# Kernel tuning notes

Measured on AMD Instinct MI355X. Metric: run time of the kernel, lower is better.

Reference implementation:

```python
import jax, jax.numpy as jnp
import numpy as np

B, S, D_MODEL = 2, 2048, 1024
H, D = 16, 64
D_INNER = H * D
EPS = 1e-5


def setup_inputs() -> dict:
    key = jax.random.key(0)
    ks = jax.random.split(key, 10)
    sc = 0.02
    return {
        "x": jax.random.normal(ks[0], (B, S, D_MODEL), dtype=jnp.float32),
        "Wq": jax.random.normal(ks[1], (D_MODEL, D_INNER), dtype=jnp.float32) * sc,
        "Wk": jax.random.normal(ks[2], (D_MODEL, D_INNER), dtype=jnp.float32) * sc,
        "Wv": jax.random.normal(ks[3], (D_MODEL, D_INNER), dtype=jnp.float32) * sc,
        "Wg": jax.random.normal(ks[4], (D_MODEL, D_INNER), dtype=jnp.float32) * sc,
        "Wa": jax.random.normal(ks[5], (D_MODEL, H), dtype=jnp.float32) * sc,
        "ba": jax.random.normal(ks[6], (H,), dtype=jnp.float32) * sc,
        "Wo": jax.random.normal(ks[7], (D_INNER, D_MODEL), dtype=jnp.float32) * sc,
        "gn_w": jnp.ones((D_INNER,), dtype=jnp.float32),
        "gn_b": jnp.zeros((D_INNER,), dtype=jnp.float32),
    }


def reference(x, Wq, Wk, Wv, Wg, Wa, ba, Wo, gn_w, gn_b):
    b, s, _ = x.shape
    # projections -> [B,H,S,D]
    q = jax.nn.silu(jnp.einsum('bsm,md->bsd', x, Wq).reshape(b, s, H, D).transpose(0, 2, 1, 3))
    k = jax.nn.silu(jnp.einsum('bsm,md->bsd', x, Wk).reshape(b, s, H, D).transpose(0, 2, 1, 3))
    v = jnp.einsum('bsm,md->bsd', x, Wv).reshape(b, s, H, D).transpose(0, 2, 1, 3)

    # data-dependent log forget gate, per head: [B,H,S]
    log_alpha = -jax.nn.softplus(jnp.einsum('bsm,mh->bsh', x, Wa) + ba)
    cum = jnp.cumsum(log_alpha, axis=1).transpose(0, 2, 1)  # [B,H,S]

    # decay[b,h,i,j] = exp(cum[i] - cum[j]) for j <= i, else 0
    diff = cum[:, :, :, None] - cum[:, :, None, :]  # [B,H,S,S]
    causal = jnp.tril(jnp.ones((s, s), dtype=bool))
    decay = jnp.exp(jnp.where(causal, diff, -jnp.inf))

    attn = jnp.einsum('bhid,bhjd->bhij', q, k) * decay
    o = jnp.einsum('bhij,bhjd->bhid', attn, v)  # [B,H,S,D]
    o = o.transpose(0, 2, 1, 3)  # [B,S,H,D]

    # GroupNorm(H groups) over channels-within-group and spatial dim S
    mean = jnp.mean(o, axis=(1, 3), keepdims=True)          # per (b,h)
    var = jnp.var(o, axis=(1, 3), keepdims=True)
    o = (o - mean) / jnp.sqrt(var + EPS)
    o = o * gn_w.reshape(H, D) + gn_b.reshape(H, D)
    o = o.reshape(b, s, H * D)

    gate = jax.nn.sigmoid(jnp.einsum('bsm,md->bsd', x, Wg))
    return jnp.einsum('bsd,dm->bsm', o * gate, Wo)
```

## Files before the change

kernel.cpp:

```cpp
#include <hip/hip_runtime.h>
#include <math.h>
#include <stdint.h>

typedef __attribute__((ext_vector_type(4))) float f32x4;
typedef __attribute__((ext_vector_type(8))) short bf16x8;

constexpr int NB = 2;
constexpr int NS = 2048;
constexpr int NM = 1024;
constexpr int NH = 16;
constexpr int ND = 64;
constexpr int NDI = 1024;

__device__ __forceinline__ float bf2f(unsigned short u) {
  uint32_t x = ((uint32_t)u) << 16; float f; __builtin_memcpy(&f, &x, 4); return f;
}
__device__ __forceinline__ unsigned short f2bf(float f) {
  uint32_t x; __builtin_memcpy(&x, &f, 4);
  x += 0x7FFFu + ((x >> 16) & 1u);
  return (unsigned short)(x >> 16);
}

__global__ __launch_bounds__(256) void k_prep(const float* __restrict__ x,
    const float* __restrict__ w0, const float* __restrict__ w1,
    const float* __restrict__ w2, const float* __restrict__ w3,
    const float* __restrict__ w4, const float* __restrict__ Wa,
    unsigned short* __restrict__ xb,
    unsigned short* __restrict__ t0, unsigned short* __restrict__ t1,
    unsigned short* __restrict__ t2, unsigned short* __restrict__ t3,
    unsigned short* __restrict__ t4, unsigned short* __restrict__ wa_pad) {
  int bid = blockIdx.x;
  if (bid < 2048) {
    int i = bid * 256 + threadIdx.x;
    const float4* p = (const float4*)(x + (size_t)i * 8);
    float4 a = p[0], b = p[1];
    unsigned short r[8] = {f2bf(a.x), f2bf(a.y), f2bf(a.z), f2bf(a.w),
                           f2bf(b.x), f2bf(b.y), f2bf(b.z), f2bf(b.w)};
    *(uint4*)(xb + (size_t)i * 8) = *(const uint4*)r;
  } else if (bid < 7168) {
    __shared__ float tile[32][33];
    int w = bid - 2048;
    int z = w >> 10, within = w & 1023;
    const float* src = z == 0 ? w0 : z == 1 ? w1 : z == 2 ? w2 : z == 3 ? w3 : w4;
    unsigned short* dst = z == 0 ? t0 : z == 1 ? t1 : z == 2 ? t2 : z == 3 ? t3 : t4;
    int c0 = (within & 31) * 32, r0 = (within >> 5) * 32;
    int tx = threadIdx.x & 31, ty = threadIdx.x >> 5;
    #pragma unroll
    for (int i = 0; i < 4; i++)
      tile[ty + i * 8][tx] = src[(size_t)(r0 + ty + i * 8) * 1024 + c0 + tx];
    __syncthreads();
    #pragma unroll
    for (int i = 0; i < 4; i++)
      dst[(size_t)(c0 + ty + i * 8) * 1024 + r0 + tx] = f2bf(tile[tx][ty + i * 8]);
  } else {
    int idx = (bid - 7168) * 256 + threadIdx.x;
    int h = idx >> 10, k2 = idx & 1023;
    wa_pad[idx] = (h < 16) ? f2bf(Wa[k2 * 16 + h]) : (unsigned short)0;
  }
}

__global__ __launch_bounds__(256) void k_la_gemm(const unsigned short* __restrict__ xb,
    const unsigned short* __restrict__ wa_pad, float* __restrict__ la8) {
  __shared__ unsigned short As[128 * 32];
  __shared__ unsigned short Bs[128 * 32];
  int tid = threadIdx.x;
  int row0 = blockIdx.y * 128;
  int kbeg = blockIdx.x * 128;
  float* Cp = la8 + (size_t)blockIdx.x * (32 * 2048);
  int w = tid >> 6, l = tid & 63;
  int wr = w >> 1, wc = w & 1;
  int lr = l & 15, lk = l >> 4;
  f32x4 acc[4] = {};
  for (int k0 = kbeg; k0 < kbeg + 128; k0 += 32) {
    __syncthreads();
    #pragma unroll
    for (int i = 0; i < 2; i++) {
      int idx = tid + i * 256;
      int r = idx >> 2, c = idx & 3;
      int cs = c ^ ((r >> 1) & 3);
      const unsigned short* srcA = xb + (size_t)(row0 + r) * NM + k0 + cs * 8;
      const unsigned short* srcB = wa_pad + (size_t)r * NM + k0 + cs * 8;
      __builtin_amdgcn_global_load_lds(
          (const __attribute__((address_space(1))) void*)srcA,
          (__attribute__((address_space(3))) void*)((char*)As + (w * 64 + i * 256) * 16),
          16, 0, 0);
      __builtin_amdgcn_global_load_lds(
          (const __attribute__((address_space(1))) void*)srcB,
          (__attribute__((address_space(3))) void*)((char*)Bs + (w * 64 + i * 256) * 16),
          16, 0, 0);
    }
    __syncthreads();
    if (wc == 0) {
      bf16x8 b = *(const bf16x8*)&Bs[lr * 32 + (lk ^ ((lr >> 1) & 3)) * 8];
      #pragma unroll
      for (int m = 0; m < 4; m++) {
        int ra = wr * 64 + m * 16 + lr;
        bf16x8 a = *(const bf16x8*)&As[ra * 32 + (lk ^ ((ra >> 1) & 3)) * 8];
        acc[m] = __builtin_amdgcn_mfma_f32_16x16x32_bf16(a, b, acc[m], 0, 0, 0);
      }
    }
  }
  if (wc == 0) {
    #pragma unroll
    for (int m = 0; m < 4; m++) {
      #pragma unroll
      for (int j = 0; j < 4; j++) {
        int row = row0 + wr * 64 + m * 16 + lk * 4 + j;
        int bb = row >> 11, s = row & 2047;
        Cp[((size_t)(bb * 16 + lr)) * 2048 + s] = acc[m][j];
      }
    }
  }
}

__global__ __launch_bounds__(256) void k_cumsum(const float* __restrict__ la8,
    const float* __restrict__ ba, float* __restrict__ cum,
    float* __restrict__ psum, float* __restrict__ psq) {
  int g = blockIdx.x;
  int h = g & 15;
  if (threadIdx.x == 0) { psum[g] = 0.f; psq[g] = 0.f; }
  float bah = ba[h];
  const float* p0 = la8 + (size_t)g * NS;
  float* out = cum + (size_t)g * NS;
  __shared__ float part[256];
  float v[8]; float sum = 0.f;
  int base = threadIdx.x * 8;
  #pragma unroll
  for (int i = 0; i < 8; i++) {
    int s = base + i;
    float z = bah;
    #pragma unroll
    for (int sl = 0; sl < 8; sl++) z += p0[sl * 65536 + s];
    float sp = fmaxf(z, 0.f) + log1pf(expf(-fabsf(z)));
    v[i] = -sp; sum += v[i];
  }
  part[threadIdx.x] = sum;
  __syncthreads();
  for (int off = 1; off < 256; off <<= 1) {
    float add = (threadIdx.x >= off) ? part[threadIdx.x - off] : 0.f;
    __syncthreads();
    part[threadIdx.x] += add;
    __syncthreads();
  }
  float run = (threadIdx.x > 0) ? part[threadIdx.x - 1] : 0.f;
  #pragma unroll
  for (int i = 0; i < 8; i++) { run += v[i]; out[base + i] = run; }
}

__global__ __launch_bounds__(512, 2) void k_proj8(
    const unsigned short* __restrict__ A,
    const unsigned short* __restrict__ Wcat,
    unsigned short* __restrict__ q, unsigned short* __restrict__ k,
    unsigned short* __restrict__ v, unsigned short* __restrict__ g) {
  __shared__ unsigned short Ab[2][256 * 64];
  __shared__ unsigned short Bb[2][256 * 64];
  int tid = threadIdx.x;
  int bid = blockIdx.x;
  int wg = (bid & 7) * 32 + (bid >> 3);
  int bx = wg & 15, by = wg >> 4;
  int row0 = by * 256, col0 = bx * 256;
  int wid = tid >> 6, lane = tid & 63;
  int WR = wid >> 2, WC = wid & 3;
  int lr = lane & 15, lk = lane >> 4;

  auto stage = [&](int kt, int bi) {
    #pragma unroll
    for (int i = 0; i < 4; i++) {
      int idx = tid + i * 512;
      int r = idx >> 3, c = idx & 7;
      int cs = c ^ (r & 7);
      const unsigned short* srcA = A + (size_t)(row0 + r) * NM + kt * 64 + cs * 8;
      __builtin_amdgcn_global_load_lds(
          (const __attribute__((address_space(1))) void*)srcA,
          (__attribute__((address_space(3))) void*)((char*)&Ab[bi][0] + (wid * 64 + i * 512) * 16),
          16, 0, 0);
      const unsigned short* srcB = Wcat + (size_t)(col0 + r) * NM + kt * 64 + cs * 8;
      __builtin_amdgcn_global_load_lds(
          (const __attribute__((address_space(1))) void*)srcB,
          (__attribute__((address_space(3))) void*)((char*)&Bb[bi][0] + (wid * 64 + i * 512) * 16),
          16, 0, 0);
    }
  };

  stage(0, 0);
  stage(1, 1);

  f32x4 acc[8][4] = {};
  for (int kt = 0; kt < 16; ++kt) {
    int bi = kt & 1;
    if (kt < 15) asm volatile("s_waitcnt vmcnt(8)" ::: "memory");
    else         asm volatile("s_waitcnt vmcnt(0)" ::: "memory");
    __builtin_amdgcn_sched_barrier(0);
    __builtin_amdgcn_s_barrier();

    const char* Ap = (const char*)&Ab[bi][0];
    const char* Bp = (const char*)&Bb[bi][0];
    bf16x8 a0[8], b0[4], a1[8], b1[4];
    #pragma unroll
    for (int m = 0; m < 8; m++) {
      int r = WR * 128 + m * 16 + lr;
      a0[m] = *(const bf16x8*)(Ap + r * 128 + ((lk ^ (r & 7)) * 16));
    }
    #pragma unroll
    for (int n = 0; n < 4; n++) {
      int r = WC * 64 + n * 16 + lr;
      b0[n] = *(const bf16x8*)(Bp + r * 128 + ((lk ^ (r & 7)) * 16));
    }
    #pragma unroll
    for (int m = 0; m < 8; m++)
      #pragma unroll
      for (int n = 0; n < 4; n++)
        acc[m][n] = __builtin_amdgcn_mfma_f32_16x16x32_bf16(a0[m], b0[n], acc[m][n], 0, 0, 0);
    #pragma unroll
    for (int m = 0; m < 8; m++) {
      int r = WR * 128 + m * 16 + lr;
      a1[m] = *(const bf16x8*)(Ap + r * 128 + (((lk + 4) ^ (r & 7)) * 16));
    }
    #pragma unroll
    for (int n = 0; n < 4; n++) {
      int r = WC * 64 + n * 16 + lr;
      b1[n] = *(const bf16x8*)(Bp + r * 128 + (((lk + 4) ^ (r & 7)) * 16));
    }
    asm volatile("s_waitcnt lgkmcnt(0)" ::: "memory");
    __builtin_amdgcn_sched_barrier(0);
    __builtin_amdgcn_s_barrier();
    if (kt + 2 < 16) stage(kt + 2, bi);
    __builtin_amdgcn_s_setprio(1);
    #pragma unroll
    for (int m = 0; m < 8; m++)
      #pragma unroll
      for (int n = 0; n < 4; n++)
        acc[m][n] = __builtin_amdgcn_mfma_f32_16x16x32_bf16(a1[m], b1[n], acc[m][n], 0, 0, 0);
    __builtin_amdgcn_s_setprio(0);
  }

  #pragma unroll
  for (int m = 0; m < 8; m++) {
    #pragma unroll
    for (int n = 0; n < 4; n++) {
      int col = col0 + WC * 64 + n * 16 + lr;
      int zone = col >> 10;
      unsigned short* dst = zone == 0 ? q : zone == 1 ? k : zone == 2 ? v : g;
      int cb = col & 1023;
      #pragma unroll
      for (int j = 0; j < 4; j++) {
        int row = row0 + WR * 128 + m * 16 + lk * 4 + j;
        float val = acc[m][n][j];
        if (zone <= 1) val = val / (1.f + expf(-val));
        else if (zone == 3) val = 1.f / (1.f + expf(-val));
        dst[(size_t)row * 1024 + cb] = f2bf(val);
      }
    }
  }
}

__global__ __launch_bounds__(256) void k_out2(const unsigned short* __restrict__ A,
    const unsigned short* __restrict__ Bt, float* __restrict__ C) {
  __shared__ unsigned short As[2][64 * 64];
  __shared__ unsigned short Bs[2][128 * 64];
  int tid = threadIdx.x;
  int bid = blockIdx.x;
  int wg = (bid & 7) * 64 + (bid >> 3);
  int bx = wg & 7, by = wg >> 3;
  int row0 = by * 64, col0 = bx * 128;
  int w = tid >> 6, l = tid & 63;
  int wr = w >> 1, wc = w & 1;
  int lr = l & 15, lk = l >> 4;

  auto stage = [&](int t, int bi) {
    #pragma unroll
    for (int i = 0; i < 2; i++) {
      int idx = tid + i * 256;
      int r = idx >> 3, c = idx & 7;
      int cs = c ^ (r & 7);
      const unsigned short* srcA = A + (size_t)(row0 + r) * NM + t * 64 + cs * 8;
      __builtin_amdgcn_global_load_lds(
          (const __attribute__((address_space(1))) void*)srcA,
          (__attribute__((address_space(3))) void*)((char*)&As[bi][0] + idx * 16),
          16, 0, 0);
    }
    #pragma unroll
    for (int i = 0; i < 4; i++) {
      int idx = tid + i * 256;
      int r = idx >> 3, c = idx & 7;
      int cs = c ^ (r & 7);
      const unsigned short* srcB = Bt + (size_t)(col0 + r) * NM + t * 64 + cs * 8;
      __builtin_amdgcn_global_load_lds(
          (const __attribute__((address_space(1))) void*)srcB,
          (__attribute__((address_space(3))) void*)((char*)&Bs[bi][0] + idx * 16),
          16, 0, 0);
    }
  };

  stage(0, 0);
  asm volatile("s_waitcnt vmcnt(0)" ::: "memory");
  __builtin_amdgcn_s_barrier();

  f32x4 acc[2][4] = {};
  int cur = 0;
  for (int t = 0; t < 16; ++t) {
    if (t < 15) stage(t + 1, cur ^ 1);
    const char* Ap = (const char*)&As[cur][0];
    const char* Bp = (const char*)&Bs[cur][0];
    bf16x8 a[2][2], b[4][2];
    #pragma unroll
    for (int m = 0; m < 2; m++) {
      int ra = wr * 32 + m * 16 + lr;
      #pragma unroll
      for (int kk = 0; kk < 2; kk++)
        a[m][kk] = *(const bf16x8*)(Ap + ra * 128 + (((kk * 4 + lk) ^ (ra & 7)) * 16));
    }
    #pragma unroll
    for (int n = 0; n < 4; n++) {
      int rb = wc * 64 + n * 16 + lr;
      #pragma unroll
      for (int kk = 0; kk < 2; kk++)
        b[n][kk] = *(const bf16x8*)(Bp + rb * 128 + (((kk * 4 + lk) ^ (rb & 7)) * 16));
    }
    __builtin_amdgcn_s_setprio(1);
    #pragma unroll
    for (int kk = 0; kk < 2; kk++)
      #pragma unroll
      for (int m = 0; m < 2; m++)
        #pragma unroll
        for (int n = 0; n < 4; n++)
          acc[m][n] = __builtin_amdgcn_mfma_f32_16x16x32_bf16(a[m][kk], b[n][kk], acc[m][n], 0, 0, 0);
    __builtin_amdgcn_s_setprio(0);
    asm volatile("s_waitcnt vmcnt(0)" ::: "memory");
    __builtin_amdgcn_s_barrier();
    cur ^= 1;
  }
  #pragma unroll
  for (int m = 0; m < 2; m++)
    #pragma unroll
    for (int n = 0; n < 4; n++)
      #pragma unroll
      for (int j = 0; j < 4; j++) {
        int row = row0 + wr * 32 + m * 16 + lk * 4 + j;
        int col = col0 + wc * 64 + n * 16 + lr;
        C[(size_t)row * NM + col] = acc[m][n][j];
      }
}

__global__ __launch_bounds__(256) void k_attn(const unsigned short* __restrict__ q,
    const unsigned short* __restrict__ kk, const unsigned short* __restrict__ vv,
    const float* __restrict__ cum, unsigned short* __restrict__ o,
    float* __restrict__ psum, float* __restrict__ psq) {
  int it = blockIdx.x, h = blockIdx.y, b = blockIdx.z;
  int i0 = it * 64;
  __shared__ unsigned short Qs[64 * 64];
  __shared__ unsigned short Ks[64 * 64];
  __shared__ unsigned short Ps[64 * 64];
  __shared__ unsigned short Vt[64 * 66];
  __shared__ float ci[64], cj[64];
  __shared__ int jlo_s;
  int tid = threadIdx.x;
  int w = tid >> 6, lane = tid & 63;
  int cl = lane & 15, hi = lane >> 4;
  const size_t hb = (size_t)b * NS * NDI + (size_t)h * ND;
  const float* cumh = cum + (size_t)(b * NH + h) * NS;

  #pragma unroll
  for (int lp = 0; lp < 2; lp++) {
    int idx = tid + lp * 256;
    int r = idx >> 3, cb = (idx & 7) * 16;
    uint4 t = *(const uint4*)(q + hb + (size_t)(i0 + r) * NDI + (cb >> 1));
    *(uint4*)((char*)Qs + r * 128 + (cb ^ ((r & 7) << 4))) = t;
  }
  if (tid < 64) ci[tid] = cumh[i0 + tid];
  if (tid < 64) {
    int jt = tid;
    bool ok = (jt <= it) && (cumh[i0] - cumh[jt * 64 + 63] >= -25.f);
    unsigned long long mask = __ballot(ok);
    if (tid == 0) jlo_s = (int)__builtin_ctzll(mask);
  }
  __syncthreads();
  int jlo = jlo_s;

  int arow = w * 16 + cl;
  int xr = (cl & 7) << 4;
  const char* Qb = (const char*)Qs + arow * 128;
  const char* Pb = (const char*)Ps + arow * 128;
  f32x4 acco[4] = {};

  uint4 tK[2], tV[2];
  auto gload = [&](int j0) {
    #pragma unroll
    for (int lp = 0; lp < 2; lp++) {
      int idx = tid + lp * 256;
      int r = idx >> 3, c8h = (idx & 7) * 8;
      tK[lp] = *(const uint4*)(kk + hb + (size_t)(j0 + r) * NDI + c8h);
      tV[lp] = *(const uint4*)(vv + hb + (size_t)(j0 + r) * NDI + c8h);
    }
  };
  if (jlo <= it) gload(jlo * 64);

  for (int jt = jlo; jt <= it; jt++) {
    int j0 = jt * 64;
    __syncthreads();
    if (tid < 64) cj[tid] = cumh[j0 + tid];
    #pragma unroll
    for (int lp = 0; lp < 2; lp++) {
      int idx = tid + lp * 256;
      int r = idx >> 3, cb = (idx & 7) * 16;
      *(uint4*)((char*)Ks + r * 128 + (cb ^ ((r & 7) << 4))) = tK[lp];
      unsigned short us[8]; *(uint4*)us = tV[lp];
      int c8 = (idx & 7) * 8;
      #pragma unroll
      for (int e = 0; e < 8; e++) Vt[(c8 + e) * 66 + r] = us[e];
    }
    if (jt + 1 <= it) gload(j0 + 64);
    __syncthreads();
    bf16x8 a0 = *(const bf16x8*)(Qb + ((hi * 16) ^ xr));
    bf16x8 a1 = *(const bf16x8*)(Qb + ((64 + hi * 16) ^ xr));
    f32x4 accs[4] = {};
    #pragma unroll
    for (int jtile = 0; jtile < 4; jtile++) {
      const char* Kb = (const char*)Ks + (jtile * 16 + cl) * 128;
      bf16x8 b0 = *(const bf16x8*)(Kb + ((hi * 16) ^ xr));
      bf16x8 b1 = *(const bf16x8*)(Kb + ((64 + hi * 16) ^ xr));
      accs[jtile] = __builtin_amdgcn_mfma_f32_16x16x32_bf16(a0, b0, accs[jtile], 0, 0, 0);
      accs[jtile] = __builtin_amdgcn_mfma_f32_16x16x32_bf16(a1, b1, accs[jtile], 0, 0, 0);
    }
    #pragma unroll
    for (int jtile = 0; jtile < 4; jtile++) {
      #pragma unroll
      for (int reg = 0; reg < 4; reg++) {
        int irl = w * 16 + hi * 4 + reg;
        int jl = jtile * 16 + cl;
        float dec = ((j0 + jl) <= (i0 + irl)) ? __expf(ci[irl] - cj[jl]) : 0.f;
        float pv = accs[jtile][reg] * dec;
        *(unsigned short*)((char*)Ps + irl * 128 + ((2 * jl) ^ ((irl & 7) << 4))) = f2bf(pv);
      }
    }
    __syncthreads();
    #pragma unroll
    for (int kk2 = 0; kk2 < 2; kk2++) {
      bf16x8 pa = *(const bf16x8*)(Pb + ((kk2 * 64 + hi * 16) ^ xr));
      #pragma unroll
      for (int dt = 0; dt < 4; dt++) {
        const unsigned int* vp = (const unsigned int*)(Vt + (dt * 16 + cl) * 66 + kk2 * 32 + hi * 8);
        uint4 tmp;
        tmp.x = vp[0]; tmp.y = vp[1]; tmp.z = vp[2]; tmp.w = vp[3];
        bf16x8 vb = *(const bf16x8*)&tmp;
        acco[dt] = __builtin_amdgcn_mfma_f32_16x16x32_bf16(pa, vb, acco[dt], 0, 0, 0);
      }
    }
  }
  #pragma unroll
  for (int dt = 0; dt < 4; dt++) {
    #pragma unroll
    for (int reg = 0; reg < 4; reg++) {
      int row = i0 + w * 16 + hi * 4 + reg;
      o[hb + (size_t)row * NDI + dt * 16 + cl] = f2bf(acco[dt][reg]);
    }
  }
  float sm = 0.f, sq = 0.f;
  #pragma unroll
  for (int dt = 0; dt < 4; dt++)
    #pragma unroll
    for (int reg = 0; reg < 4; reg++) { float t2 = acco[dt][reg]; sm += t2; sq += t2 * t2; }
  #pragma unroll
  for (int off = 32; off > 0; off >>= 1) {
    sm += __shfl_down(sm, off, 64);
    sq += __shfl_down(sq, off, 64);
  }
  __syncthreads();
  float* ws2 = (float*)Ps;
  if (lane == 0) { ws2[w * 2] = sm; ws2[w * 2 + 1] = sq; }
  __syncthreads();
  if (tid == 0) {
    float S = 0.f, Q2 = 0.f;
    #pragma unroll
    for (int i = 0; i < 4; i++) { S += ws2[i * 2]; Q2 += ws2[i * 2 + 1]; }
    atomicAdd(&psum[b * NH + h], S);
    atomicAdd(&psq[b * NH + h], Q2);
  }
}

__global__ __launch_bounds__(256) void k_gate(const unsigned short* __restrict__ o,
    const unsigned short* __restrict__ gsig, const float* __restrict__ psum,
    const float* __restrict__ psq, const float* __restrict__ gnw,
    const float* __restrict__ gnb, unsigned short* __restrict__ u) {
  int idx4 = blockIdx.x * 256 + threadIdx.x;
  size_t base = (size_t)idx4 * 4;
  int c = (int)(base & (NDI - 1));
  int row = (int)(base >> 10);
  int b = row >> 11;
  int h = c >> 6;
  int g = b * NH + h;
  float n = (float)(NS * ND);
  float mean = psum[g] / n;
  float var = psq[g] / n - mean * mean;
  float rstd = rsqrtf(var + 1e-5f);
  ushort4 ov = *(const ushort4*)(o + base);
  ushort4 gv = *(const ushort4*)(gsig + base);
  float4 w4 = *(const float4*)(gnw + c);
  float4 b4 = *(const float4*)(gnb + c);
  unsigned short r[4];
  r[0] = f2bf(((bf2f(ov.x) - mean) * rstd * w4.x + b4.x) * bf2f(gv.x));
  r[1] = f2bf(((bf2f(ov.y) - mean) * rstd * w4.y + b4.y) * bf2f(gv.y));
  r[2] = f2bf(((bf2f(ov.z) - mean) * rstd * w4.z + b4.z) * bf2f(gv.z));
  r[3] = f2bf(((bf2f(ov.w) - mean) * rstd * w4.w + b4.w) * bf2f(gv.w));
  *(ushort4*)(u + base) = *(const ushort4*)r;
}

extern "C" void kernel_launch(void* const* d_in, const int* in_sizes, int n_in,
                              void* d_out, int out_size, void* d_ws, size_t ws_size,
                              hipStream_t stream) {
  const float* x   = (const float*)d_in[0];
  const float* Wq  = (const float*)d_in[1];
  const float* Wk  = (const float*)d_in[2];
  const float* Wv  = (const float*)d_in[3];
  const float* Wg  = (const float*)d_in[4];
  const float* Wa  = (const float*)d_in[5];
  const float* ba  = (const float*)d_in[6];
  const float* Wo  = (const float*)d_in[7];
  const float* gnw = (const float*)d_in[8];
  const float* gnb = (const float*)d_in[9];
  float* out = (float*)d_out;

  const size_t NTOK = (size_t)NB * NS;
  char* p = (char*)d_ws;
  float* la8 = (float*)p;                 p += (size_t)8 * 32 * NS * 4;
  float* cum = (float*)p;                 p += (size_t)NB * NH * NS * 4;
  float* psum = (float*)p;                p += 32 * 4;
  float* psq  = (float*)p;                p += 32 * 4;
  p = (char*)(((uintptr_t)p + 255) & ~(uintptr_t)255);
  unsigned short* xb   = (unsigned short*)p; p += NTOK * NM * 2;
  unsigned short* Wcat = (unsigned short*)p; p += (size_t)4 * NM * NDI * 2;
  unsigned short* wto  = (unsigned short*)p; p += (size_t)NDI * NM * 2;
  unsigned short* wa_pad = (unsigned short*)p; p += (size_t)128 * NM * 2;
  unsigned short* q  = (unsigned short*)p;  p += NTOK * NDI * 2;
  unsigned short* k  = (unsigned short*)p;  p += NTOK * NDI * 2;
  unsigned short* v  = (unsigned short*)p;  p += NTOK * NDI * 2;
  unsigned short* g  = (unsigned short*)p;  p += NTOK * NDI * 2;
  unsigned short* u  = (unsigned short*)p;  p += NTOK * NDI * 2;
  unsigned short* o  = (unsigned short*)p;  p += NTOK * NDI * 2;

  unsigned short* wtq = Wcat;
  unsigned short* wtk = Wcat + (size_t)NM * NDI;
  unsigned short* wtv = Wcat + (size_t)2 * NM * NDI;
  unsigned short* wtg = Wcat + (size_t)3 * NM * NDI;

  k_prep    <<<dim3(7680), 256, 0, stream>>>(x, Wq, Wk, Wv, Wg, Wo, Wa,
                                             xb, wtq, wtk, wtv, wtg, wto, wa_pad);
  k_la_gemm <<<dim3(8, 32), 256, 0, stream>>>(xb, wa_pad, la8);
  k_cumsum  <<<dim3(NB * NH), 256, 0, stream>>>(la8, ba, cum, psum, psq);
  k_proj8   <<<dim3(256), 512, 0, stream>>>(xb, Wcat, q, k, v, g);
  k_attn    <<<dim3(32, NH, NB), 256, 0, stream>>>(q, k, v, cum, o, psum, psq);
  k_gate    <<<dim3(4096), 256, 0, stream>>>(o, g, psum, psq, gnw, gnb, u);
  k_out2    <<<dim3(512), 256, 0, stream>>>(u, wto, out);
}
```

Before: 119.0 us.

## Fuse GroupNorm and sigmoid gating into output projection GEMM A-tile staging

Removes the separate k_gate elementwise kernel and the intermediate u buffer. The output GEMM now loads o and the gate tiles into registers, applies the GroupNorm normalization, affine transform and gate multiply, and writes the bf16 result into LDS as the A operand. This saves a kernel launch and a full round trip of the gated activations through global memory. In exchange the GEMM's A-tile path moves from async global-to-LDS loads to register loads plus ALU work, and the tile must be written before the barrier, which may expose latency.

```diff
diff --git a/kernel.cpp b/kernel.cpp
--- a/kernel.cpp
+++ b/kernel.cpp
@@ -254,10 +254,14 @@
   }
 }
 
-__global__ __launch_bounds__(256) void k_out2(const unsigned short* __restrict__ A,
-    const unsigned short* __restrict__ Bt, float* __restrict__ C) {
+__global__ __launch_bounds__(256) void k_out2f(const unsigned short* __restrict__ o,
+    const unsigned short* __restrict__ gsig, const float* __restrict__ psum,
+    const float* __restrict__ psq, const float* __restrict__ gnw,
+    const float* __restrict__ gnb, const unsigned short* __restrict__ Bt,
+    float* __restrict__ C) {
   __shared__ unsigned short As[2][64 * 64];
   __shared__ unsigned short Bs[2][128 * 64];
+  __shared__ float sstat[32][2];
   int tid = threadIdx.x;
   int bid = blockIdx.x;
   int wg = (bid & 7) * 64 + (bid >> 3);
@@ -267,18 +271,15 @@
   int wr = w >> 1, wc = w & 1;
   int lr = l & 15, lk = l >> 4;
 
-  auto stage = [&](int t, int bi) {
-    #pragma unroll
-    for (int i = 0; i < 2; i++) {
-      int idx = tid + i * 256;
-      int r = idx >> 3, c = idx & 7;
-      int cs = c ^ (r & 7);
-      const unsigned short* srcA = A + (size_t)(row0 + r) * NM + t * 64 + cs * 8;
-      __builtin_amdgcn_global_load_lds(
-          (const __attribute__((address_space(1))) void*)srcA,
-          (__attribute__((address_space(3))) void*)((char*)&As[bi][0] + idx * 16),
-          16, 0, 0);
-    }
+  if (tid < 32) {
+    float n = (float)(NS * ND);
+    float mean = psum[tid] / n;
+    float var = psq[tid] / n - mean * mean;
+    sstat[tid][0] = mean;
+    sstat[tid][1] = rsqrtf(var + 1e-5f);
+  }
+
+  auto stageB = [&](int t, int bi) {
     #pragma unroll
     for (int i = 0; i < 4; i++) {
       int idx = tid + i * 256;
@@ -291,15 +292,55 @@
           16, 0, 0);
     }
   };
-
-  stage(0, 0);
+  uint4 tO[2], tG[2];
+  auto loadA = [&](int t) {
+    #pragma unroll
+    for (int i = 0; i < 2; i++) {
+      int idx = tid + i * 256;
+      int r = idx >> 3, c = idx & 7;
+      int cs = c ^ (r & 7);
+      size_t off = (size_t)(row0 + r) * NM + t * 64 + cs * 8;
+      tO[i] = *(const uint4*)(o + off);
+      tG[i] = *(const uint4*)(gsig + off);
+    }
+  };
+  auto writeA = [&](int t, int bi) {
+    #pragma unroll
+    for (int i = 0; i < 2; i++) {
+      int idx = tid + i * 256;
+      int r = idx >> 3, c = idx & 7;
+      int cs = c ^ (r & 7);
+      int row = row0 + r;
+      int cb = t * 64 + cs * 8;
+      int gidx = (row >> 11) * NH + (cb >> 6);
+      float mean = sstat[gidx][0], rstd = sstat[gidx][1];
+      float4 w0 = *(const float4*)(gnw + cb);
+      float4 w1 = *(const float4*)(gnw + cb + 4);
+      float4 b0 = *(const float4*)(gnb + cb);
+      float4 b1 = *(const float4*)(gnb + cb + 4);
+      float wv[8] = {w0.x, w0.y, w0.z, w0.w, w1.x, w1.y, w1.z, w1.w};
+      float bv[8] = {b0.x, b0.y, b0.z, b0.w, b1.x, b1.y, b1.z, b1.w};
+      unsigned short ob[8], gb[8], ub[8];
+      *(uint4*)ob = tO[i]; *(uint4*)gb = tG[i];
+      #pragma unroll
+      for (int e = 0; e < 8; e++)
+        ub[e] = f2bf(((bf2f(ob[e]) - mean) * rstd * wv[e] + bv[e]) * bf2f(gb[e]));
+      *(uint4*)((char*)&As[bi][0] + idx * 16) = *(const uint4*)ub;
+    }
+  };
+
+  stageB(0, 0);
+  loadA(0);
   asm volatile("s_waitcnt vmcnt(0)" ::: "memory");
+  __syncthreads();
+  writeA(0, 0);
+  asm volatile("s_waitcnt lgkmcnt(0)" ::: "memory");
   __builtin_amdgcn_s_barrier();
 
   f32x4 acc[2][4] = {};
   int cur = 0;
   for (int t = 0; t < 16; ++t) {
-    if (t < 15) stage(t + 1, cur ^ 1);
+    if (t < 15) { stageB(t + 1, cur ^ 1); loadA(t + 1); }
     const char* Ap = (const char*)&As[cur][0];
     const char* Bp = (const char*)&Bs[cur][0];
     bf16x8 a[2][2], b[4][2];
@@ -327,6 +368,9 @@
           acc[m][n] = __builtin_amdgcn_mfma_f32_16x16x32_bf16(a[m][kk], b[n][kk], acc[m][n], 0, 0, 0);
     __builtin_amdgcn_s_setprio(0);
     asm volatile("s_waitcnt vmcnt(0)" ::: "memory");
+    if (t < 15) writeA(t + 1, cur ^ 1);
+    asm volatile("s_waitcnt lgkmcnt(0)" ::: "memory");
+    __builtin_amdgcn_sched_barrier(0);
     __builtin_amdgcn_s_barrier();
     cur ^= 1;
   }
@@ -478,33 +522,6 @@
   }
 }
 
-__global__ __launch_bounds__(256) void k_gate(const unsigned short* __restrict__ o,
-    const unsigned short* __restrict__ gsig, const float* __restrict__ psum,
-    const float* __restrict__ psq, const float* __restrict__ gnw,
-    const float* __restrict__ gnb, unsigned short* __restrict__ u) {
-  int idx4 = blockIdx.x * 256 + threadIdx.x;
-  size_t base = (size_t)idx4 * 4;
-  int c = (int)(base & (NDI - 1));
-  int row = (int)(base >> 10);
-  int b = row >> 11;
-  int h = c >> 6;
-  int g = b * NH + h;
-  float n = (float)(NS * ND);
-  float mean = psum[g] / n;
-  float var = psq[g] / n - mean * mean;
-  float rstd = rsqrtf(var + 1e-5f);
-  ushort4 ov = *(const ushort4*)(o + base);
-  ushort4 gv = *(const ushort4*)(gsig + base);
-  float4 w4 = *(const float4*)(gnw + c);
-  float4 b4 = *(const float4*)(gnb + c);
-  unsigned short r[4];
-  r[0] = f2bf(((bf2f(ov.x) - mean) * rstd * w4.x + b4.x) * bf2f(gv.x));
-  r[1] = f2bf(((bf2f(ov.y) - mean) * rstd * w4.y + b4.y) * bf2f(gv.y));
-  r[2] = f2bf(((bf2f(ov.z) - mean) * rstd * w4.z + b4.z) * bf2f(gv.z));
-  r[3] = f2bf(((bf2f(ov.w) - mean) * rstd * w4.w + b4.w) * bf2f(gv.w));
-  *(ushort4*)(u + base) = *(const ushort4*)r;
-}
-
 extern "C" void kernel_launch(void* const* d_in, const int* in_sizes, int n_in,
                               void* d_out, int out_size, void* d_ws, size_t ws_size,
                               hipStream_t stream) {
@@ -535,7 +552,6 @@
   unsigned short* k  = (unsigned short*)p;  p += NTOK * NDI * 2;
   unsigned short* v  = (unsigned short*)p;  p += NTOK * NDI * 2;
   unsigned short* g  = (unsigned short*)p;  p += NTOK * NDI * 2;
-  unsigned short* u  = (unsigned short*)p;  p += NTOK * NDI * 2;
   unsigned short* o  = (unsigned short*)p;  p += NTOK * NDI * 2;
 
   unsigned short* wtq = Wcat;
@@ -549,6 +565,5 @@
   k_cumsum  <<<dim3(NB * NH), 256, 0, stream>>>(la8, ba, cum, psum, psq);
   k_proj8   <<<dim3(256), 512, 0, stream>>>(xb, Wcat, q, k, v, g);
   k_attn    <<<dim3(32, NH, NB), 256, 0, stream>>>(q, k, v, cum, o, psum, psq);
-  k_gate    <<<dim3(4096), 256, 0, stream>>>(o, g, psum, psq, gnw, gnb, u);
-  k_out2    <<<dim3(512), 256, 0, stream>>>(u, wto, out);
-}
+  k_out2f   <<<dim3(512), 256, 0, stream>>>(o, g, psum, psq, gnw, gnb, wto, out);
+}
```

After: 123.8 us. 1.04x slower.
